# Kernel tuning notes

Hardware: AMD Instinct MI355X
Metric: run time of the kernel (lower is better)

Reference implementation:

```python
import jax, jax.numpy as jnp
import numpy as np

L, H, D, DH, DFF, V, P, T, R = 12, 12, 768, 64, 3072, 30522, 512, 2, 50
RAT_LAYER = 6  # original condition: 5 < idx < 7


def layer_norm(x, g, b, eps=1e-12):
    m = x.mean(-1, keepdims=True)
    v = ((x - m) ** 2).mean(-1, keepdims=True)
    return (x - m) / jnp.sqrt(v + eps) * g + b


def setup_inputs() -> dict:
    key = jax.random.key(0)
    ks = iter(jax.random.split(key, 20))
    def n(shape, s=0.02):
        return jax.random.normal(next(ks), shape, dtype=jnp.float32) * s
    inp = dict(
        input_ids=jax.random.randint(next(ks), (4, 512), 0, V, dtype=jnp.int32),
        relations=jax.random.randint(next(ks), (4, 512, 512), 0, R, dtype=jnp.int32),
        attention_mask=jnp.ones((4, 512), dtype=jnp.int32),
        word_emb=n((V, D)), pos_emb=n((P, D)), type_emb=n((T, D)),
        emb_ln_g=jnp.ones((D,)), emb_ln_b=jnp.zeros((D,)),
        Wq=n((L, D, D)), bq=jnp.zeros((L, D)), Wk=n((L, D, D)), bk=jnp.zeros((L, D)),
        Wv=n((L, D, D)), bv=jnp.zeros((L, D)), Wo=n((L, D, D)), bo=jnp.zeros((L, D)),
        ln1_g=jnp.ones((L, D)), ln1_b=jnp.zeros((L, D)),
        Wi=n((L, D, DFF)), bi=jnp.zeros((L, DFF)),
        Wf=n((L, DFF, D)), bf=jnp.zeros((L, D)),
        ln2_g=jnp.ones((L, D)), ln2_b=jnp.zeros((L, D)),
        key_rel=n((L, R, DH)), val_rel=n((L, R, DH)),
        pool_w=n((D, D)), pool_b=jnp.zeros((D,)),
    )
    return inp


def reference(input_ids, relations, attention_mask, word_emb, pos_emb, type_emb,
              emb_ln_g, emb_ln_b, Wq, bq, Wk, bk, Wv, bv, Wo, bo, ln1_g, ln1_b,
              Wi, bi, Wf, bf, ln2_g, ln2_b, key_rel, val_rel, pool_w, pool_b):
    B, S = input_ids.shape
    # BERT embeddings (token_type_ids = zeros as in module default)
    h = word_emb[input_ids] + pos_emb[jnp.arange(S)][None] + type_emb[0][None, None]
    h = layer_norm(h, emb_ln_g, emb_ln_b)
    ext_mask = (1.0 - attention_mask.astype(jnp.float32))[:, None, None, :] * -10000.0
    inv_sqrt_dh = np.float32(1.0 / np.sqrt(DH))
    for i in range(L):
        q = (h @ Wq[i] + bq[i]).reshape(B, S, H, DH).transpose(0, 2, 1, 3)
        k = (h @ Wk[i] + bk[i]).reshape(B, S, H, DH).transpose(0, 2, 1, 3)
        v = (h @ Wv[i] + bv[i]).reshape(B, S, H, DH).transpose(0, 2, 1, 3)
        scores = jnp.einsum('bhsd,bhtd->bhst', q, k)
        if i == RAT_LAYER:
            kr = key_rel[i][relations]            # [B,S,S,DH] gathered relation keys
            scores = scores + jnp.einsum('bhsd,bstd->bhst', q, kr)
        scores = scores * inv_sqrt_dh + ext_mask
        probs = jax.nn.softmax(scores, axis=-1)   # dropout = identity (eval)
        ctx = jnp.einsum('bhst,bhtd->bhsd', probs, v)
        if i == RAT_LAYER:
            vr = val_rel[i][relations]            # [B,S,S,DH] gathered relation values
            ctx = ctx + jnp.einsum('bhst,bstd->bhsd', probs, vr)
        ctx = ctx.transpose(0, 2, 1, 3).reshape(B, S, D)
        attn_out = layer_norm(ctx @ Wo[i] + bo[i] + h, ln1_g[i], ln1_b[i])
        ff = jax.nn.gelu(attn_out @ Wi[i] + bi[i], approximate=False)
        h = layer_norm(ff @ Wf[i] + bf[i] + attn_out, ln2_g[i], ln2_b[i])
    pooled = jnp.tanh(h[:, 0] @ pool_w + pool_b)
    return h, pooled
```

## Files before the change

kernel.cpp:

```cpp
#include <hip/hip_runtime.h>
#include <math.h>

typedef unsigned short u16;
typedef unsigned int   u32;
typedef __bf16  bf16x8 __attribute__((ext_vector_type(8)));
typedef float   f32x4  __attribute__((ext_vector_type(4)));
typedef u16     u16x8  __attribute__((ext_vector_type(8)));

__device__ __forceinline__ u16 f2bf(float f) {
  u32 u = __builtin_bit_cast(u32, f);
  u32 r = (u + 0x7fffu + ((u >> 16) & 1u)) >> 16;
  return (u16)r;
}
__device__ __forceinline__ float bf2f(u16 h) {
  u32 u = ((u32)h) << 16;
  return __builtin_bit_cast(float, u);
}
__device__ __forceinline__ void gload16(const void* g, void* l) {
  __builtin_amdgcn_global_load_lds((const __attribute__((address_space(1))) void*)g,
                                   (__attribute__((address_space(3))) void*)l, 16, 0, 0);
}
__device__ __forceinline__ bf16x8 ld_bf8(const u16* p) {
  u16x8 v = *(const u16x8*)p;
  return __builtin_bit_cast(bf16x8, v);
}
__device__ __forceinline__ f32x4 mfma16(bf16x8 a, bf16x8 b, f32x4 c) {
  return __builtin_amdgcn_mfma_f32_16x16x32_bf16(a, b, c, 0, 0, 0);
}

struct ConvP {
  const float *wq, *wk, *wv, *wo, *wi, *wf;
  u16 *oqkv, *oo, *oi, *of;
};
__global__ __launch_bounds__(256) void conv_weights(ConvP p) {
  int t = blockIdx.x;
  const float* in; u16* out; int K, N, tn, tk;
  if (t < 1728) { int wh = t / 576, tt = t % 576;
    in = wh==0 ? p.wq : (wh==1 ? p.wk : p.wv);
    out = p.oqkv + (size_t)wh * 768 * 768;
    K = 768; N = 768; tn = tt % 24; tk = tt / 24;
  } else if (t < 2304) { int tt = t - 1728; in = p.wo; out = p.oo; K=768;  N=768;  tn=tt%24; tk=tt/24; }
  else if (t < 4608)   { int tt = t - 2304; in = p.wi; out = p.oi; K=768;  N=3072; tn=tt%96; tk=tt/96; }
  else                 { int tt = t - 4608; in = p.wf; out = p.of; K=3072; N=768;  tn=tt%24; tk=tt/24; }
  int n0 = tn*32, k0 = tk*32;
  __shared__ float tile[32][33];
  int x = threadIdx.x, y = threadIdx.y;
  #pragma unroll
  for (int j = 0; j < 4; ++j)
    tile[y + j*8][x] = in[(size_t)(k0 + y + j*8) * N + n0 + x];
  __syncthreads();
  #pragma unroll
  for (int j = 0; j < 4; ++j)
    out[(size_t)(n0 + y + j*8) * K + k0 + x] = f2bf(tile[x][y + j*8]);
}

struct GP {
  const u16* A; const u16* B;
  int K, N;
  long sA, sB, sOut;
  const float* bias; const float* res;
  float* outF; u16* outB;
  const float* bq; const float* bk; const float* bv;
  u16* qO; u16* kO; u16* vO;
};

template<int BM, int BN, int WAVES, int EPI, int KS>
__global__ __launch_bounds__(WAVES*64) void gemm_bt(GP p) {
  constexpr int THREADS = WAVES * 64;
  constexpr int WC = WAVES / 2;
  constexpr int WM = BM / 2, WN = BN / WC, MR = WM / 16, NR = WN / 16;
  constexpr int AIT = BM * 64 / (THREADS * 8);
  constexpr int BIT = BN * 64 / (THREADS * 8);
  const int tid = threadIdx.x;
  const int wave = tid >> 6, lane = tid & 63;
  const int wr = wave / WC, wc = wave % WC;
  const int wm0 = wr * WM, wn0 = wc * WN;
  const int bn = blockIdx.x, bm = blockIdx.y, bz = blockIdx.z;
  const int K = p.K;
  const int kLen = K / KS;
  const int kBeg = (KS > 1) ? bz * kLen : 0;
  const u16* A  = p.A + ((KS > 1) ? 0 : (size_t)bz * p.sA);
  const u16* Bp = p.B + ((KS > 1) ? 0 : (size_t)bz * p.sB);
  const int rowA0 = bm * BM, colB0 = bn * BN;

  __shared__ __align__(16) u16 lds[(BM + BN) * 64];
  u16* Al = lds; u16* Bl = lds + BM * 64;

  f32x4 acc[MR][NR];
  #pragma unroll
  for (int i = 0; i < MR; ++i)
    #pragma unroll
    for (int j = 0; j < NR; ++j) acc[i][j] = f32x4{0.f,0.f,0.f,0.f};

  for (int kt = kBeg; kt < kBeg + kLen; kt += 64) {
    #pragma unroll
    for (int it = 0; it < AIT; ++it) {
      int e = tid * 8 + it * THREADS * 8;
      gload16(A + (size_t)(rowA0 + (e >> 6)) * K + kt + (e & 63), Al + e);
    }
    #pragma unroll
    for (int it = 0; it < BIT; ++it) {
      int e = tid * 8 + it * THREADS * 8;
      gload16(Bp + (size_t)(colB0 + (e >> 6)) * K + kt + (e & 63), Bl + e);
    }
    __syncthreads();
    #pragma unroll
    for (int ks = 0; ks < 2; ++ks) {
      bf16x8 av[MR]; bf16x8 bw[NR];
      #pragma unroll
      for (int mf = 0; mf < MR; ++mf)
        av[mf] = ld_bf8(Al + (wm0 + mf*16 + (lane&15))*64 + ks*32 + (lane>>4)*8);
      #pragma unroll
      for (int nf = 0; nf < NR; ++nf)
        bw[nf] = ld_bf8(Bl + (wn0 + nf*16 + (lane&15))*64 + ks*32 + (lane>>4)*8);
      #pragma unroll
      for (int mf = 0; mf < MR; ++mf)
        #pragma unroll
        for (int nf = 0; nf < NR; ++nf)
          acc[mf][nf] = mfma16(av[mf], bw[nf], acc[mf][nf]);
    }
    __syncthreads();
  }

  #pragma unroll
  for (int mf = 0; mf < MR; ++mf) {
    #pragma unroll
    for (int nf = 0; nf < NR; ++nf) {
      int col = colB0 + wn0 + nf*16 + (lane & 15);
      #pragma unroll
      for (int reg = 0; reg < 4; ++reg) {
        int row = rowA0 + wm0 + mf*16 + (lane >> 4)*4 + reg;
        float v = acc[mf][nf][reg];
        if constexpr (EPI == 0) {
          int wh = col / 768, cc = col % 768;
          int hh = cc >> 6, d = col & 63;
          int b = row >> 9, s = row & 511;
          const float* bias = wh==0 ? p.bq : (wh==1 ? p.bk : p.bv);
          u16 o = f2bf(v + bias[cc]);
          if (wh == 0)      p.qO[((((size_t)b*12 + hh)*512 + s) << 6) + d] = o;
          else if (wh == 1) p.kO[((((size_t)b*12 + hh)*512 + s) << 6) + d] = o;
          else              p.vO[((((size_t)b*12 + hh)*64  + d) << 9) + s] = o;
        } else if constexpr (EPI == 1) {
          int b = bz / 12, hh = bz % 12;
          p.outB[((size_t)(b*512 + row))*768 + hh*64 + col] = f2bf(v);
        } else if constexpr (EPI == 2) {
          p.outF[(size_t)bz * p.sOut + (size_t)row * p.N + col] = v;
        } else {
          float xg = v + p.bias[col];
          float gg = 0.5f * xg * (1.f + erff(xg * 0.70710678118f));
          p.outB[(size_t)row * p.N + col] = f2bf(gg);
        }
      }
    }
  }
}

__global__ __launch_bounds__(256) void attn_scores(
    const u16* __restrict__ q, const u16* __restrict__ k,
    const int* __restrict__ mask, u16* __restrict__ probs,
    const float* __restrict__ qr, const int* __restrict__ rel,
    float* __restrict__ wbins, int rat) {
  int st = blockIdx.x, hh = blockIdx.y, b = blockIdx.z;
  int tid = threadIdx.x, wave = tid >> 6, lane = tid & 63;
  size_t bh = (size_t)b * 12 + hh;
  const u16* qb = q + bh * 512 * 64;
  const u16* kb = k + bh * 512 * 64;

  f32x4 acc[2][8];
  #pragma unroll
  for (int i = 0; i < 2; ++i)
    #pragma unroll
    for (int j = 0; j < 8; ++j) acc[i][j] = f32x4{0.f,0.f,0.f,0.f};

  #pragma unroll
  for (int ks = 0; ks < 2; ++ks) {
    bf16x8 a0 = ld_bf8(qb + (size_t)(st*32      + (lane&15))*64 + ks*32 + (lane>>4)*8);
    bf16x8 a1 = ld_bf8(qb + (size_t)(st*32 + 16 + (lane&15))*64 + ks*32 + (lane>>4)*8);
    #pragma unroll
    for (int nf = 0; nf < 8; ++nf) {
      int t = wave*128 + nf*16 + (lane&15);
      bf16x8 bb = ld_bf8(kb + (size_t)t*64 + ks*32 + (lane>>4)*8);
      acc[0][nf] = mfma16(a0, bb, acc[0][nf]);
      acc[1][nf] = mfma16(a1, bb, acc[1][nf]);
    }
  }

  __shared__ float qlds[32][52];
  __shared__ float wlds[32][52];
  if (rat) {
    for (int i = tid; i < 32*52; i += 256) ((float*)wlds)[i] = 0.f;
    for (int i = tid; i < 32*50; i += 256) {
      int rr = i % 50, sr = i / 50;
      qlds[sr][rr] = qr[(bh*512 + st*32 + sr)*50 + rr];
    }
    __syncthreads();
    #pragma unroll
    for (int mf = 0; mf < 2; ++mf)
      #pragma unroll
      for (int nf = 0; nf < 8; ++nf) {
        int t = wave*128 + nf*16 + (lane&15);
        #pragma unroll
        for (int reg = 0; reg < 4; ++reg) {
          int rl = mf*16 + (lane>>4)*4 + reg;
          int rr = rel[((size_t)b*512 + st*32 + rl)*512 + t];
          acc[mf][nf][reg] += qlds[rl][rr];
        }
      }
  }

  #pragma unroll
  for (int nf = 0; nf < 8; ++nf) {
    int t = wave*128 + nf*16 + (lane&15);
    float em = -10000.f * (1.f - (float)mask[b*512 + t]);
    #pragma unroll
    for (int mf = 0; mf < 2; ++mf)
      #pragma unroll
      for (int reg = 0; reg < 4; ++reg)
        acc[mf][nf][reg] = acc[mf][nf][reg] * 0.125f + em;
  }

  __shared__ float red[4][32];
  __shared__ float gval[32];

  float rmax[2][4];
  #pragma unroll
  for (int mf = 0; mf < 2; ++mf)
    #pragma unroll
    for (int reg = 0; reg < 4; ++reg) {
      float m = -3.4e38f;
      #pragma unroll
      for (int nf = 0; nf < 8; ++nf) m = fmaxf(m, acc[mf][nf][reg]);
      #pragma unroll
      for (int o = 1; o < 16; o <<= 1) m = fmaxf(m, __shfl_xor(m, o));
      rmax[mf][reg] = m;
    }
  if ((lane & 15) == 0) {
    #pragma unroll
    for (int mf = 0; mf < 2; ++mf)
      #pragma unroll
      for (int reg = 0; reg < 4; ++reg)
        red[wave][mf*16 + (lane>>4)*4 + reg] = rmax[mf][reg];
  }
  __syncthreads();
  if (tid < 32)
    gval[tid] = fmaxf(fmaxf(red[0][tid], red[1][tid]), fmaxf(red[2][tid], red[3][tid]));
  __syncthreads();

  float rsum[2][4] = {{0,0,0,0},{0,0,0,0}};
  #pragma unroll
  for (int mf = 0; mf < 2; ++mf)
    #pragma unroll
    for (int reg = 0; reg < 4; ++reg) {
      int rl = mf*16 + (lane>>4)*4 + reg;
      float gm = gval[rl];
      #pragma unroll
      for (int nf = 0; nf < 8; ++nf) {
        float pv = __expf(acc[mf][nf][reg] - gm);
        acc[mf][nf][reg] = pv;
        rsum[mf][reg] += pv;
      }
    }
  #pragma unroll
  for (int mf = 0; mf < 2; ++mf)
    #pragma unroll
    for (int reg = 0; reg < 4; ++reg)
      #pragma unroll
      for (int o = 1; o < 16; o <<= 1) rsum[mf][reg] += __shfl_xor(rsum[mf][reg], o);
  __syncthreads();
  if ((lane & 15) == 0) {
    #pragma unroll
    for (int mf = 0; mf < 2; ++mf)
      #pragma unroll
      for (int reg = 0; reg < 4; ++reg)
        red[wave][mf*16 + (lane>>4)*4 + reg] = rsum[mf][reg];
  }
  __syncthreads();
  if (tid < 32)
    gval[tid] = red[0][tid] + red[1][tid] + red[2][tid] + red[3][tid];
  __syncthreads();

  #pragma unroll
  for (int mf = 0; mf < 2; ++mf)
    #pragma unroll
    for (int reg = 0; reg < 4; ++reg) {
      int rl = mf*16 + (lane>>4)*4 + reg;
      float inv = 1.f / gval[rl];
      size_t rowbase = (bh*512 + st*32 + rl) * 512;
      #pragma unroll
      for (int nf = 0; nf < 8; ++nf) {
        int t = wave*128 + nf*16 + (lane&15);
        float pval = acc[mf][nf][reg] * inv;
        probs[rowbase + t] = f2bf(pval);
        if (rat) {
          int rr = rel[((size_t)b*512 + st*32 + rl)*512 + t];
          atomicAdd(&wlds[rl][rr], pval);
        }
      }
    }
  if (rat) {
    __syncthreads();
    for (int i = tid; i < 32*50; i += 256) {
      int rr = i % 50, sr = i / 50;
      wbins[(bh*512 + st*32 + sr)*50 + rr] = wlds[sr][rr];
    }
  }
}

__global__ __launch_bounds__(256) void rat_qr(const u16* __restrict__ q,
    const float* __restrict__ kr, float* __restrict__ qr) {
  int idx = blockIdx.x * 256 + threadIdx.x;
  if (idx >= 24576 * 50) return;
  int r = idx % 50; size_t bhs = (size_t)idx / 50;
  const u16* qp = q + bhs * 64;
  const float* kp = kr + r * 64;
  float acc = 0.f;
  #pragma unroll
  for (int d = 0; d < 64; ++d) acc += bf2f(qp[d]) * kp[d];
  qr[idx] = acc;
}

__global__ __launch_bounds__(256) void rat_apply(const float* __restrict__ wbins,
    const float* __restrict__ vr, u16* __restrict__ ctx) {
  __shared__ float vrl[50*64];
  __shared__ float wl[32*50];
  int tid = threadIdx.x;
  int rows0 = blockIdx.x * 32;
  for (int i = tid; i < 50*64; i += 256) vrl[i] = vr[i];
  for (int i = tid; i < 32*50; i += 256) wl[i] = wbins[(size_t)rows0*50 + i];
  __syncthreads();
  int wave = tid >> 6, lane = tid & 63;
  #pragma unroll
  for (int i = 0; i < 8; ++i) {
    int r = wave*8 + i;
    size_t idx = (size_t)rows0 + r;
    float acc = 0.f;
    #pragma unroll
    for (int j = 0; j < 50; ++j) acc += wl[r*50 + j] * vrl[j*64 + lane];
    int s = (int)(idx & 511); size_t bh = idx >> 9;
    int b = (int)(bh / 12), hh = (int)(bh % 12);
    u16* cp = ctx + ((size_t)(b*512 + s))*768 + hh*64 + lane;
    *cp = f2bf(bf2f(*cp) + acc);
  }
}

__global__ __launch_bounds__(256) void embed_ln(const int* __restrict__ ids,
    const float* __restrict__ we, const float* __restrict__ pe, const float* __restrict__ te,
    const float* __restrict__ g, const float* __restrict__ b,
    float* __restrict__ hF, u16* __restrict__ hB) {
  int row = blockIdx.x, tid = threadIdx.x;
  int s = row & 511;
  int id = ids[row];
  float x[3];
  #pragma unroll
  for (int j = 0; j < 3; ++j) {
    int d = tid + j*256;
    x[j] = we[(size_t)id*768 + d] + pe[(size_t)s*768 + d] + te[d];
  }
  __shared__ float red[4];
  float sm = x[0] + x[1] + x[2];
  #pragma unroll
  for (int o = 32; o; o >>= 1) sm += __shfl_xor(sm, o);
  if (!(tid & 63)) red[tid >> 6] = sm;
  __syncthreads();
  float mean = (red[0]+red[1]+red[2]+red[3]) * (1.f/768.f);
  __syncthreads();
  float q = 0.f;
  #pragma unroll
  for (int j = 0; j < 3; ++j) { float d = x[j] - mean; q += d*d; }
  #pragma unroll
  for (int o = 32; o; o >>= 1) q += __shfl_xor(q, o);
  if (!(tid & 63)) red[tid >> 6] = q;
  __syncthreads();
  float inv = rsqrtf((red[0]+red[1]+red[2]+red[3]) * (1.f/768.f) + 1e-12f);
  #pragma unroll
  for (int j = 0; j < 3; ++j) {
    int d = tid + j*256;
    float y = (x[j] - mean) * inv * g[d] + b[d];
    hF[(size_t)row*768 + d] = y;
    hB[(size_t)row*768 + d] = f2bf(y);
  }
}

__global__ __launch_bounds__(256) void ln_fused(const float* __restrict__ p0,
    const float* __restrict__ p1, const float* __restrict__ p2, const float* __restrict__ p3,
    int np, const float* __restrict__ bias, const float* __restrict__ res,
    const float* __restrict__ g, const float* __restrict__ b,
    float* __restrict__ oF, u16* __restrict__ oB) {
  int row = blockIdx.x, tid = threadIdx.x;
  size_t base = (size_t)row * 768;
  float v[3];
  #pragma unroll
  for (int j = 0; j < 3; ++j) {
    int d = tid + j*256;
    float x = p0[base + d];
    if (np > 1) x += p1[base + d];
    if (np > 2) x += p2[base + d];
    if (np > 3) x += p3[base + d];
    v[j] = x + bias[d] + res[base + d];
  }
  __shared__ float red[4];
  float sm = v[0] + v[1] + v[2];
  #pragma unroll
  for (int o = 32; o; o >>= 1) sm += __shfl_xor(sm, o);
  if (!(tid & 63)) red[tid >> 6] = sm;
  __syncthreads();
  float mean = (red[0]+red[1]+red[2]+red[3]) * (1.f/768.f);
  __syncthreads();
  float q = 0.f;
  #pragma unroll
  for (int j = 0; j < 3; ++j) { float d = v[j] - mean; q += d*d; }
  #pragma unroll
  for (int o = 32; o; o >>= 1) q += __shfl_xor(q, o);
  if (!(tid & 63)) red[tid >> 6] = q;
  __syncthreads();
  float inv = rsqrtf((red[0]+red[1]+red[2]+red[3]) * (1.f/768.f) + 1e-12f);
  #pragma unroll
  for (int j = 0; j < 3; ++j) {
    int d = tid + j*256;
    float y = (v[j] - mean) * inv * g[d] + b[d];
    oF[base + d] = y;
    oB[base + d] = f2bf(y);
  }
}

__global__ __launch_bounds__(256) void pooler_k(const float* __restrict__ h,
    const float* __restrict__ w, const float* __restrict__ bias, float* __restrict__ out) {
  int b = blockIdx.x, tid = threadIdx.x;
  __shared__ float hr[768];
  for (int i = tid; i < 768; i += 256) hr[i] = h[((size_t)b*512)*768 + i];
  __syncthreads();
  float a0 = 0.f, a1 = 0.f, a2 = 0.f;
  for (int kk = 0; kk < 768; ++kk) {
    float hv = hr[kk];
    const float* wr = w + (size_t)kk*768;
    a0 += hv * wr[tid]; a1 += hv * wr[tid+256]; a2 += hv * wr[tid+512];
  }
  out[(size_t)b*768 + tid]       = tanhf(a0 + bias[tid]);
  out[(size_t)b*768 + tid + 256] = tanhf(a1 + bias[tid+256]);
  out[(size_t)b*768 + tid + 512] = tanhf(a2 + bias[tid+512]);
}

__global__ __launch_bounds__(256) void copy_out(const float* __restrict__ in, float* __restrict__ out) {
  size_t i = ((size_t)blockIdx.x * 256 + threadIdx.x) * 4;
  *(float4*)(out + i) = *(const float4*)(in + i);
}

extern "C" void kernel_launch(void* const* d_in, const int* in_sizes, int n_in,
                              void* d_out, int out_size, void* d_ws, size_t ws_size,
                              hipStream_t stream) {
  const int*   ids   = (const int*)d_in[0];
  const int*   rel   = (const int*)d_in[1];
  const int*   amask = (const int*)d_in[2];
  const float* we    = (const float*)d_in[3];
  const float* pe    = (const float*)d_in[4];
  const float* te    = (const float*)d_in[5];
  const float* eg    = (const float*)d_in[6];
  const float* ebb   = (const float*)d_in[7];
  const float* Wq    = (const float*)d_in[8];
  const float* bq    = (const float*)d_in[9];
  const float* Wk    = (const float*)d_in[10];
  const float* bk    = (const float*)d_in[11];
  const float* Wv    = (const float*)d_in[12];
  const float* bv    = (const float*)d_in[13];
  const float* Wo    = (const float*)d_in[14];
  const float* bo    = (const float*)d_in[15];
  const float* g1    = (const float*)d_in[16];
  const float* b1    = (const float*)d_in[17];
  const float* Wi    = (const float*)d_in[18];
  const float* bi    = (const float*)d_in[19];
  const float* Wf    = (const float*)d_in[20];
  const float* bfp   = (const float*)d_in[21];
  const float* g2    = (const float*)d_in[22];
  const float* b2    = (const float*)d_in[23];
  const float* krel  = (const float*)d_in[24];
  const float* vrel  = (const float*)d_in[25];
  const float* pwp   = (const float*)d_in[26];
  const float* pbp   = (const float*)d_in[27];
  (void)in_sizes; (void)n_in; (void)out_size; (void)ws_size;

  char* ws = (char*)d_ws;
  size_t off = 0;
  auto take = [&](size_t bytes) { char* p = ws + off; off += (bytes + 255) & ~(size_t)255; return p; };
  u16*   wqkv = (u16*)take((size_t)2304*768*2);
  u16*   wo_l = (u16*)take((size_t)768*768*2);
  u16*   wi_l = (u16*)take((size_t)3072*768*2);
  u16*   wf_l = (u16*)take((size_t)768*3072*2);
  float* hF   = (float*)take((size_t)2048*768*4);
  u16*   hB   = (u16*)take((size_t)2048*768*2);
  float* atF  = (float*)take((size_t)2048*768*4);
  u16*   atB  = (u16*)take((size_t)2048*768*2);
  u16*   qB   = (u16*)take((size_t)2048*768*2);
  u16*   kB   = (u16*)take((size_t)2048*768*2);
  u16*   vB   = (u16*)take((size_t)2048*768*2);
  u16*   ctxB = (u16*)take((size_t)2048*768*2);
  float* tmpF = (float*)take((size_t)4*2048*768*4);
  u16*   ffB  = (u16*)take((size_t)2048*3072*2);
  u16*   prB  = (u16*)take((size_t)48*512*512*2);
  float* qrF  = (float*)take((size_t)24576*50*4);
  float* wbF  = (float*)take((size_t)24576*50*4);
  const size_t PSTRIDE = (size_t)2048*768;

  embed_ln<<<2048, 256, 0, stream>>>(ids, we, pe, te, eg, ebb, hF, hB);

  for (int l = 0; l < 12; ++l) {
    ConvP cp{Wq + (size_t)l*768*768, Wk + (size_t)l*768*768, Wv + (size_t)l*768*768,
             Wo + (size_t)l*768*768, Wi + (size_t)l*768*3072, Wf + (size_t)l*3072*768,
             wqkv, wo_l, wi_l, wf_l};
    conv_weights<<<6912, dim3(32,8), 0, stream>>>(cp);

    GP pq{}; pq.A = hB; pq.B = wqkv; pq.K = 768; pq.N = 2304;
    pq.bq = bq + l*768; pq.bk = bk + l*768; pq.bv = bv + l*768;
    pq.qO = qB; pq.kO = kB; pq.vO = vB;
    gemm_bt<128,128,8,0,1><<<dim3(18,16,1), 512, 0, stream>>>(pq);

    int rat = (l == 6) ? 1 : 0;
    if (rat) rat_qr<<<4800, 256, 0, stream>>>(qB, krel + 6*50*64, qrF);
    attn_scores<<<dim3(16,12,4), 256, 0, stream>>>(qB, kB, amask, prB, qrF, rel, wbF, rat);

    GP pc{}; pc.A = prB; pc.B = vB; pc.K = 512; pc.N = 64;
    pc.sA = 512*512; pc.sB = 64*512; pc.outB = ctxB;
    gemm_bt<64,64,4,1,1><<<dim3(1,8,48), 256, 0, stream>>>(pc);
    if (rat) rat_apply<<<768, 256, 0, stream>>>(wbF, vrel + 6*50*64, ctxB);

    GP po{}; po.A = ctxB; po.B = wo_l; po.K = 768; po.N = 768; po.sOut = PSTRIDE;
    po.outF = tmpF;
    gemm_bt<64,128,4,2,2><<<dim3(6,32,2), 256, 0, stream>>>(po);
    ln_fused<<<2048, 256, 0, stream>>>(tmpF, tmpF + PSTRIDE, nullptr, nullptr, 2,
                                       bo + l*768, hF, g1 + l*768, b1 + l*768, atF, atB);

    GP pf1{}; pf1.A = atB; pf1.B = wi_l; pf1.K = 768; pf1.N = 3072;
    pf1.bias = bi + (size_t)l*3072; pf1.outB = ffB;
    gemm_bt<128,128,8,3,1><<<dim3(24,16,1), 512, 0, stream>>>(pf1);

    GP pf2{}; pf2.A = ffB; pf2.B = wf_l; pf2.K = 3072; pf2.N = 768; pf2.sOut = PSTRIDE;
    pf2.outF = tmpF;
    gemm_bt<64,128,4,2,4><<<dim3(6,32,4), 256, 0, stream>>>(pf2);
    ln_fused<<<2048, 256, 0, stream>>>(tmpF, tmpF + PSTRIDE, tmpF + 2*PSTRIDE, tmpF + 3*PSTRIDE, 4,
                                       bfp + l*768, atF, g2 + l*768, b2 + l*768, hF, hB);
  }

  copy_out<<<1536, 256, 0, stream>>>(hF, (float*)d_out);
  pooler_k<<<4, 256, 0, stream>>>(hF, pwp, pbp, (float*)d_out + (size_t)2048*768);
}
```

Measured before the change: 2.009 ms.

## Fuse probs@V into attention scores kernel, keeping probabilities in LDS

The attention kernel now stages each block's normalized 32x512 probability tile in LDS as bf16 and immediately computes the P·V product with MFMA, writing the context directly in [B,S,D] layout. This removes the global probability buffer (48x512x512 bf16) write and re-read, plus the separate batched GEMM launch. In exchange, each block uses about 33KB more LDS, which may reduce occupancy, and V is re-read from global by every row-tile block.

After: 1.984 ms. Within noise of the previous version (-1.2%).

```diff
diff --git a/kernel.cpp b/kernel.cpp
--- a/kernel.cpp
+++ b/kernel.cpp
@@ -140,9 +140,6 @@
           if (wh == 0)      p.qO[((((size_t)b*12 + hh)*512 + s) << 6) + d] = o;
           else if (wh == 1) p.kO[((((size_t)b*12 + hh)*512 + s) << 6) + d] = o;
           else              p.vO[((((size_t)b*12 + hh)*64  + d) << 9) + s] = o;
-        } else if constexpr (EPI == 1) {
-          int b = bz / 12, hh = bz % 12;
-          p.outB[((size_t)(b*512 + row))*768 + hh*64 + col] = f2bf(v);
         } else if constexpr (EPI == 2) {
           p.outF[(size_t)bz * p.sOut + (size_t)row * p.N + col] = v;
         } else {
@@ -155,9 +152,9 @@
   }
 }
 
-__global__ __launch_bounds__(256) void attn_scores(
-    const u16* __restrict__ q, const u16* __restrict__ k,
-    const int* __restrict__ mask, u16* __restrict__ probs,
+__global__ __launch_bounds__(256) void attn_fused(
+    const u16* __restrict__ q, const u16* __restrict__ k, const u16* __restrict__ v,
+    const int* __restrict__ mask, u16* __restrict__ ctx,
     const float* __restrict__ qr, const int* __restrict__ rel,
     float* __restrict__ wbins, int rat) {
   int st = blockIdx.x, hh = blockIdx.y, b = blockIdx.z;
@@ -166,6 +163,12 @@
   const u16* qb = q + bh * 512 * 64;
   const u16* kb = k + bh * 512 * 64;
 
+  __shared__ __align__(16) u16 plds[32 * 520];
+  __shared__ float qlds[32][52];
+  __shared__ float wlds[32][52];
+  __shared__ float red[4][32];
+  __shared__ float gval[32];
+
   f32x4 acc[2][8];
   #pragma unroll
   for (int i = 0; i < 2; ++i)
@@ -185,8 +188,6 @@
     }
   }
 
-  __shared__ float qlds[32][52];
-  __shared__ float wlds[32][52];
   if (rat) {
     for (int i = tid; i < 32*52; i += 256) ((float*)wlds)[i] = 0.f;
     for (int i = tid; i < 32*50; i += 256) {
@@ -219,9 +220,6 @@
         acc[mf][nf][reg] = acc[mf][nf][reg] * 0.125f + em;
   }
 
-  __shared__ float red[4][32];
-  __shared__ float gval[32];
-
   float rmax[2][4];
   #pragma unroll
   for (int mf = 0; mf < 2; ++mf)
@@ -285,12 +283,11 @@
     for (int reg = 0; reg < 4; ++reg) {
       int rl = mf*16 + (lane>>4)*4 + reg;
       float inv = 1.f / gval[rl];
-      size_t rowbase = (bh*512 + st*32 + rl) * 512;
       #pragma unroll
       for (int nf = 0; nf < 8; ++nf) {
         int t = wave*128 + nf*16 + (lane&15);
         float pval = acc[mf][nf][reg] * inv;
-        probs[rowbase + t] = f2bf(pval);
+        plds[rl*520 + t] = f2bf(pval);
         if (rat) {
           int rr = rel[((size_t)b*512 + st*32 + rl)*512 + t];
           atomicAdd(&wlds[rl][rr], pval);
@@ -303,6 +300,30 @@
       int rr = i % 50, sr = i / 50;
       wbins[(bh*512 + st*32 + sr)*50 + rr] = wlds[sr][rr];
     }
+  }
+  __syncthreads();
+
+  const u16* vb = v + bh * 64 * 512;
+  int mt = wave >> 1, nb = wave & 1;
+  int lrow = mt*16 + (lane & 15);
+  int g = lane >> 4;
+  f32x4 c0 = f32x4{0.f,0.f,0.f,0.f}, c1 = f32x4{0.f,0.f,0.f,0.f};
+  #pragma unroll
+  for (int kt = 0; kt < 16; ++kt) {
+    bf16x8 pa = ld_bf8(plds + lrow*520 + kt*32 + g*8);
+    bf16x8 b0 = ld_bf8(vb + (size_t)(nb*16      + (lane&15))*512 + kt*32 + g*8);
+    bf16x8 b1 = ld_bf8(vb + (size_t)((nb+2)*16  + (lane&15))*512 + kt*32 + g*8);
+    c0 = mfma16(pa, b0, c0);
+    c1 = mfma16(pa, b1, c1);
+  }
+  #pragma unroll
+  for (int reg = 0; reg < 4; ++reg) {
+    int s = st*32 + mt*16 + g*4 + reg;
+    int d0 = nb*16 + (lane & 15);
+    int d1 = (nb+2)*16 + (lane & 15);
+    size_t rb = ((size_t)(b*512 + s))*768 + hh*64;
+    ctx[rb + d0] = f2bf(c0[reg]);
+    ctx[rb + d1] = f2bf(c1[reg]);
   }
 }
 
@@ -495,7 +516,6 @@
   u16*   ctxB = (u16*)take((size_t)2048*768*2);
   float* tmpF = (float*)take((size_t)4*2048*768*4);
   u16*   ffB  = (u16*)take((size_t)2048*3072*2);
-  u16*   prB  = (u16*)take((size_t)48*512*512*2);
   float* qrF  = (float*)take((size_t)24576*50*4);
   float* wbF  = (float*)take((size_t)24576*50*4);
   const size_t PSTRIDE = (size_t)2048*768;
@@ -515,11 +535,7 @@
 
     int rat = (l == 6) ? 1 : 0;
     if (rat) rat_qr<<<4800, 256, 0, stream>>>(qB, krel + 6*50*64, qrF);
-    attn_scores<<<dim3(16,12,4), 256, 0, stream>>>(qB, kB, amask, prB, qrF, rel, wbF, rat);
-
-    GP pc{}; pc.A = prB; pc.B = vB; pc.K = 512; pc.N = 64;
-    pc.sA = 512*512; pc.sB = 64*512; pc.outB = ctxB;
-    gemm_bt<64,64,4,1,1><<<dim3(1,8,48), 256, 0, stream>>>(pc);
+    attn_fused<<<dim3(16,12,4), 256, 0, stream>>>(qB, kB, vB, amask, ctxB, qrF, rel, wbF, rat);
     if (rat) rat_apply<<<768, 256, 0, stream>>>(wbF, vrel + 6*50*64, ctxB);
 
     GP po{}; po.A = ctxB; po.B = wo_l; po.K = 768; po.N = 768; po.sOut = PSTRIDE;
```

## Fuse attention scores, softmax and PV into one kernel with probs in LDS

Applied to the files above, without the earlier changes.

Replaces the separate score/softmax kernel and the batched P·V GEMM with one kernel per 64-query tile. Each wave owns 16 full rows, so the row max and sum need only a wave shuffle, and probabilities stay in LDS as bf16 instead of round-tripping a 48x512x512 global buffer. It also remaps block IDs so the tiles of one head share an XCD, and packs relation indices into registers for the RAT layer. The costs are higher register and LDS pressure per block (32 accumulator tiles, about 66KB of probs) and fewer blocks (384), which may lower occupancy.

New measurement: 2.145 ms. +6.8%, slower.

```diff
diff --git a/kernel.cpp b/kernel.cpp
--- a/kernel.cpp
+++ b/kernel.cpp
@@ -140,9 +140,6 @@
           if (wh == 0)      p.qO[((((size_t)b*12 + hh)*512 + s) << 6) + d] = o;
           else if (wh == 1) p.kO[((((size_t)b*12 + hh)*512 + s) << 6) + d] = o;
           else              p.vO[((((size_t)b*12 + hh)*64  + d) << 9) + s] = o;
-        } else if constexpr (EPI == 1) {
-          int b = bz / 12, hh = bz % 12;
-          p.outB[((size_t)(b*512 + row))*768 + hh*64 + col] = f2bf(v);
         } else if constexpr (EPI == 2) {
           p.outF[(size_t)bz * p.sOut + (size_t)row * p.N + col] = v;
         } else {
@@ -155,153 +152,139 @@
   }
 }
 
-__global__ __launch_bounds__(256) void attn_scores(
-    const u16* __restrict__ q, const u16* __restrict__ k,
-    const int* __restrict__ mask, u16* __restrict__ probs,
+template<int RAT>
+__global__ __launch_bounds__(256, RAT ? 1 : 2) void attn_fused2(
+    const u16* __restrict__ q, const u16* __restrict__ k, const u16* __restrict__ v,
+    const int* __restrict__ mask, u16* __restrict__ ctx,
     const float* __restrict__ qr, const int* __restrict__ rel,
-    float* __restrict__ wbins, int rat) {
-  int st = blockIdx.x, hh = blockIdx.y, b = blockIdx.z;
-  int tid = threadIdx.x, wave = tid >> 6, lane = tid & 63;
-  size_t bh = (size_t)b * 12 + hh;
+    float* __restrict__ wbins) {
+  const int bid = blockIdx.x;
+  const int xcd = bid & 7, slot = bid >> 3;
+  const int head = xcd * 6 + (slot >> 3);
+  const int st   = slot & 7;
+  const int b = head / 12, hh = head % 12;
+  const int tid = threadIdx.x, wave = tid >> 6, lane = tid & 63;
+  const size_t bh = (size_t)head;
   const u16* qb = q + bh * 512 * 64;
   const u16* kb = k + bh * 512 * 64;
-
-  f32x4 acc[2][8];
-  #pragma unroll
-  for (int i = 0; i < 2; ++i)
-    #pragma unroll
-    for (int j = 0; j < 8; ++j) acc[i][j] = f32x4{0.f,0.f,0.f,0.f};
-
-  #pragma unroll
-  for (int ks = 0; ks < 2; ++ks) {
-    bf16x8 a0 = ld_bf8(qb + (size_t)(st*32      + (lane&15))*64 + ks*32 + (lane>>4)*8);
-    bf16x8 a1 = ld_bf8(qb + (size_t)(st*32 + 16 + (lane&15))*64 + ks*32 + (lane>>4)*8);
-    #pragma unroll
-    for (int nf = 0; nf < 8; ++nf) {
-      int t = wave*128 + nf*16 + (lane&15);
-      bf16x8 bb = ld_bf8(kb + (size_t)t*64 + ks*32 + (lane>>4)*8);
-      acc[0][nf] = mfma16(a0, bb, acc[0][nf]);
-      acc[1][nf] = mfma16(a1, bb, acc[1][nf]);
-    }
-  }
-
-  __shared__ float qlds[32][52];
-  __shared__ float wlds[32][52];
-  if (rat) {
-    for (int i = tid; i < 32*52; i += 256) ((float*)wlds)[i] = 0.f;
-    for (int i = tid; i < 32*50; i += 256) {
+  const u16* vb = v + bh * 64 * 512;
+
+  __shared__ __align__(16) u16 plds[64 * 520];
+  __shared__ float em_lds[512];
+  __shared__ float l_lds[64];
+  extern __shared__ float dyn_unused[];
+
+  __shared__ float qlds[RAT ? 64 : 1][RAT ? 52 : 1];
+  __shared__ float wlds[RAT ? 64 : 1][RAT ? 52 : 1];
+
+  for (int i = tid; i < 512; i += 256)
+    em_lds[i] = -10000.f * (1.f - (float)mask[b*512 + i]);
+  if constexpr (RAT) {
+    for (int i = tid; i < 64*52; i += 256) ((float*)wlds)[i] = 0.f;
+    for (int i = tid; i < 64*50; i += 256) {
       int rr = i % 50, sr = i / 50;
-      qlds[sr][rr] = qr[(bh*512 + st*32 + sr)*50 + rr];
-    }
-    __syncthreads();
-    #pragma unroll
-    for (int mf = 0; mf < 2; ++mf)
+      qlds[sr][rr] = qr[(bh*512 + st*64 + sr)*50 + rr];
+    }
+  }
+  __syncthreads();
+
+  const int qrow = st*64 + wave*16 + (lane & 15);
+  bf16x8 aq0 = ld_bf8(qb + (size_t)qrow*64 +      (lane>>4)*8);
+  bf16x8 aq1 = ld_bf8(qb + (size_t)qrow*64 + 32 + (lane>>4)*8);
+
+  f32x4 acc[32];
+  #pragma unroll
+  for (int t = 0; t < 32; ++t) acc[t] = f32x4{0.f,0.f,0.f,0.f};
+
+  #pragma unroll
+  for (int t = 0; t < 32; ++t) {
+    const u16* kr = kb + (size_t)(t*16 + (lane&15))*64 + (lane>>4)*8;
+    bf16x8 b0 = ld_bf8(kr);
+    bf16x8 b1 = ld_bf8(kr + 32);
+    acc[t] = mfma16(aq0, b0, acc[t]);
+    acc[t] = mfma16(aq1, b1, acc[t]);
+  }
+
+  u32 rr4[RAT ? 32 : 1];
+  if constexpr (RAT) {
+    #pragma unroll
+    for (int t = 0; t < 32; ++t) {
+      int tt = t*16 + (lane&15);
+      u32 pack = 0;
       #pragma unroll
-      for (int nf = 0; nf < 8; ++nf) {
-        int t = wave*128 + nf*16 + (lane&15);
-        #pragma unroll
-        for (int reg = 0; reg < 4; ++reg) {
-          int rl = mf*16 + (lane>>4)*4 + reg;
-          int rr = rel[((size_t)b*512 + st*32 + rl)*512 + t];
-          acc[mf][nf][reg] += qlds[rl][rr];
-        }
+      for (int reg = 0; reg < 4; ++reg) {
+        int lq = wave*16 + (lane>>4)*4 + reg;
+        int rr = rel[((size_t)b*512 + st*64 + lq)*512 + tt];
+        pack |= (u32)rr << (8*reg);
+        acc[t][reg] += qlds[lq][rr];
       }
-  }
-
-  #pragma unroll
-  for (int nf = 0; nf < 8; ++nf) {
-    int t = wave*128 + nf*16 + (lane&15);
-    float em = -10000.f * (1.f - (float)mask[b*512 + t]);
-    #pragma unroll
-    for (int mf = 0; mf < 2; ++mf)
-      #pragma unroll
-      for (int reg = 0; reg < 4; ++reg)
-        acc[mf][nf][reg] = acc[mf][nf][reg] * 0.125f + em;
-  }
-
-  __shared__ float red[4][32];
-  __shared__ float gval[32];
-
-  float rmax[2][4];
-  #pragma unroll
-  for (int mf = 0; mf < 2; ++mf)
+      rr4[t] = pack;
+    }
+  }
+
+  #pragma unroll
+  for (int t = 0; t < 32; ++t) {
+    float em = em_lds[t*16 + (lane&15)];
+    #pragma unroll
+    for (int reg = 0; reg < 4; ++reg)
+      acc[t][reg] = acc[t][reg] * 0.125f + em;
+  }
+
+  #pragma unroll
+  for (int reg = 0; reg < 4; ++reg) {
+    const int lq = wave*16 + (lane>>4)*4 + reg;
+    float m = acc[0][reg];
+    #pragma unroll
+    for (int t = 1; t < 32; ++t) m = fmaxf(m, acc[t][reg]);
+    #pragma unroll
+    for (int o = 1; o < 16; o <<= 1) m = fmaxf(m, __shfl_xor(m, o));
+    float s = 0.f;
+    #pragma unroll
+    for (int t = 0; t < 32; ++t) {
+      float e = __expf(acc[t][reg] - m);
+      acc[t][reg] = e;
+      s += e;
+      if constexpr (RAT) {
+        int rr = (rr4[t] >> (8*reg)) & 255;
+        atomicAdd(&wlds[lq][rr], e);
+      }
+    }
+    #pragma unroll
+    for (int o = 1; o < 16; o <<= 1) s += __shfl_xor(s, o);
+    if ((lane & 15) == 0) l_lds[lq] = s;
+    float inv = 1.f / s;
+    #pragma unroll
+    for (int t = 0; t < 32; ++t)
+      plds[(size_t)lq*520 + t*16 + (lane&15)] = f2bf(acc[t][reg] * inv);
+  }
+  __syncthreads();
+
+  if constexpr (RAT) {
+    for (int i = tid; i < 64*50; i += 256) {
+      int rr = i % 50, sr = i / 50;
+      wbins[(bh*512 + st*64 + sr)*50 + rr] = wlds[sr][rr] / l_lds[sr];
+    }
+  }
+
+  f32x4 cpv[4];
+  #pragma unroll
+  for (int dt = 0; dt < 4; ++dt) cpv[dt] = f32x4{0.f,0.f,0.f,0.f};
+  #pragma unroll
+  for (int ks = 0; ks < 16; ++ks) {
+    bf16x8 pa = ld_bf8(plds + (size_t)(wave*16 + (lane&15))*520 + ks*32 + (lane>>4)*8);
+    #pragma unroll
+    for (int dt = 0; dt < 4; ++dt) {
+      bf16x8 bv_ = ld_bf8(vb + (size_t)(dt*16 + (lane&15))*512 + ks*32 + (lane>>4)*8);
+      cpv[dt] = mfma16(pa, bv_, cpv[dt]);
+    }
+  }
+  #pragma unroll
+  for (int dt = 0; dt < 4; ++dt) {
     #pragma unroll
     for (int reg = 0; reg < 4; ++reg) {
-      float m = -3.4e38f;
-      #pragma unroll
-      for (int nf = 0; nf < 8; ++nf) m = fmaxf(m, acc[mf][nf][reg]);
-      #pragma unroll
-      for (int o = 1; o < 16; o <<= 1) m = fmaxf(m, __shfl_xor(m, o));
-      rmax[mf][reg] = m;
-    }
-  if ((lane & 15) == 0) {
-    #pragma unroll
-    for (int mf = 0; mf < 2; ++mf)
-      #pragma unroll
-      for (int reg = 0; reg < 4; ++reg)
-        red[wave][mf*16 + (lane>>4)*4 + reg] = rmax[mf][reg];
-  }
-  __syncthreads();
-  if (tid < 32)
-    gval[tid] = fmaxf(fmaxf(red[0][tid], red[1][tid]), fmaxf(red[2][tid], red[3][tid]));
-  __syncthreads();
-
-  float rsum[2][4] = {{0,0,0,0},{0,0,0,0}};
-  #pragma unroll
-  for (int mf = 0; mf < 2; ++mf)
-    #pragma unroll
-    for (int reg = 0; reg < 4; ++reg) {
-      int rl = mf*16 + (lane>>4)*4 + reg;
-      float gm = gval[rl];
-      #pragma unroll
-      for (int nf = 0; nf < 8; ++nf) {
-        float pv = __expf(acc[mf][nf][reg] - gm);
-        acc[mf][nf][reg] = pv;
-        rsum[mf][reg] += pv;
-      }
-    }
-  #pragma unroll
-  for (int mf = 0; mf < 2; ++mf)
-    #pragma unroll
-    for (int reg = 0; reg < 4; ++reg)
-      #pragma unroll
-      for (int o = 1; o < 16; o <<= 1) rsum[mf][reg] += __shfl_xor(rsum[mf][reg], o);
-  __syncthreads();
-  if ((lane & 15) == 0) {
-    #pragma unroll
-    for (int mf = 0; mf < 2; ++mf)
-      #pragma unroll
-      for (int reg = 0; reg < 4; ++reg)
-        red[wave][mf*16 + (lane>>4)*4 + reg] = rsum[mf][reg];
-  }
-  __syncthreads();
-  if (tid < 32)
-    gval[tid] = red[0][tid] + red[1][tid] + red[2][tid] + red[3][tid];
-  __syncthreads();
-
-  #pragma unroll
-  for (int mf = 0; mf < 2; ++mf)
-    #pragma unroll
-    for (int reg = 0; reg < 4; ++reg) {
-      int rl = mf*16 + (lane>>4)*4 + reg;
-      float inv = 1.f / gval[rl];
-      size_t rowbase = (bh*512 + st*32 + rl) * 512;
-      #pragma unroll
-      for (int nf = 0; nf < 8; ++nf) {
-        int t = wave*128 + nf*16 + (lane&15);
-        float pval = acc[mf][nf][reg] * inv;
-        probs[rowbase + t] = f2bf(pval);
-        if (rat) {
-          int rr = rel[((size_t)b*512 + st*32 + rl)*512 + t];
-          atomicAdd(&wlds[rl][rr], pval);
-        }
-      }
-    }
-  if (rat) {
-    __syncthreads();
-    for (int i = tid; i < 32*50; i += 256) {
-      int rr = i % 50, sr = i / 50;
-      wbins[(bh*512 + st*32 + sr)*50 + rr] = wlds[sr][rr];
+      int qg = st*64 + wave*16 + (lane>>4)*4 + reg;
+      int d  = dt*16 + (lane&15);
+      ctx[((size_t)(b*512 + qg))*768 + hh*64 + d] = f2bf(cpv[dt][reg]);
     }
   }
 }
@@ -495,7 +478,6 @@
   u16*   ctxB = (u16*)take((size_t)2048*768*2);
   float* tmpF = (float*)take((size_t)4*2048*768*4);
   u16*   ffB  = (u16*)take((size_t)2048*3072*2);
-  u16*   prB  = (u16*)take((size_t)48*512*512*2);
   float* qrF  = (float*)take((size_t)24576*50*4);
   float* wbF  = (float*)take((size_t)24576*50*4);
   const size_t PSTRIDE = (size_t)2048*768;
@@ -513,14 +495,13 @@
     pq.qO = qB; pq.kO = kB; pq.vO = vB;
     gemm_bt<128,128,8,0,1><<<dim3(18,16,1), 512, 0, stream>>>(pq);
 
-    int rat = (l == 6) ? 1 : 0;
-    if (rat) rat_qr<<<4800, 256, 0, stream>>>(qB, krel + 6*50*64, qrF);
-    attn_scores<<<dim3(16,12,4), 256, 0, stream>>>(qB, kB, amask, prB, qrF, rel, wbF, rat);
-
-    GP pc{}; pc.A = prB; pc.B = vB; pc.K = 512; pc.N = 64;
-    pc.sA = 512*512; pc.sB = 64*512; pc.outB = ctxB;
-    gemm_bt<64,64,4,1,1><<<dim3(1,8,48), 256, 0, stream>>>(pc);
-    if (rat) rat_apply<<<768, 256, 0, stream>>>(wbF, vrel + 6*50*64, ctxB);
+    if (l == 6) {
+      rat_qr<<<4800, 256, 0, stream>>>(qB, krel + 6*50*64, qrF);
+      attn_fused2<1><<<384, 256, 0, stream>>>(qB, kB, vB, amask, ctxB, qrF, rel, wbF);
+      rat_apply<<<768, 256, 0, stream>>>(wbF, vrel + 6*50*64, ctxB);
+    } else {
+      attn_fused2<0><<<384, 256, 0, stream>>>(qB, kB, vB, amask, ctxB, qrF, rel, wbF);
+    }
 
     GP po{}; po.A = ctxB; po.B = wo_l; po.K = 768; po.N = 768; po.sOut = PSTRIDE;
     po.outF = tmpF;
```

## Stage Q/K tiles in LDS with 64-row blocks and templated RAT path

Applied to the files above, without the earlier changes.

The attention-scores kernel now handles 64 query rows per block instead of 32. It stages the Q tile and the full K for the head into LDS via global_load_lds, then runs the MFMAs from shared memory rather than from direct global loads. The mask bias is precomputed into LDS, and the RAT branch is a template parameter, so non-RAT layers compile without it. This cuts redundant global K reads across blocks, at the cost of about 74KB of LDS per block, which limits occupancy, and fewer blocks (384).

New measurement: 2.215 ms. 1.1x slower.

```diff
diff --git a/kernel.cpp b/kernel.cpp
--- a/kernel.cpp
+++ b/kernel.cpp
@@ -155,153 +155,160 @@
   }
 }
 
-__global__ __launch_bounds__(256) void attn_scores(
+template<int RAT>
+__global__ __launch_bounds__(256) void scores_sm(
     const u16* __restrict__ q, const u16* __restrict__ k,
     const int* __restrict__ mask, u16* __restrict__ probs,
     const float* __restrict__ qr, const int* __restrict__ rel,
-    float* __restrict__ wbins, int rat) {
-  int st = blockIdx.x, hh = blockIdx.y, b = blockIdx.z;
-  int tid = threadIdx.x, wave = tid >> 6, lane = tid & 63;
-  size_t bh = (size_t)b * 12 + hh;
-  const u16* qb = q + bh * 512 * 64;
-  const u16* kb = k + bh * 512 * 64;
-
-  f32x4 acc[2][8];
-  #pragma unroll
-  for (int i = 0; i < 2; ++i)
-    #pragma unroll
-    for (int j = 0; j < 8; ++j) acc[i][j] = f32x4{0.f,0.f,0.f,0.f};
+    float* __restrict__ wbins) {
+  const int head = blockIdx.x;
+  const int bm   = blockIdx.y;
+  const int b = head / 12;
+  const int row0 = bm * 64;
+  const int tid = threadIdx.x, wc = tid >> 6, lane = tid & 63;
+
+  __shared__ __align__(16) u16 lds[(64 + 512) * 64];
+  u16* Al = lds;
+  u16* Bl = lds + 64*64;
+  __shared__ float em_lds[512];
+  __shared__ float red[64][4];
+  __shared__ float gmax[64], gsum[64];
+
+  for (int i = tid; i < 512; i += 256)
+    em_lds[i] = -10000.f * (1.f - (float)mask[b*512 + i]);
+
+  const u16* qb = q + (size_t)head * 512 * 64;
+  const u16* kb = k + (size_t)head * 512 * 64;
+  #pragma unroll
+  for (int it = 0; it < 2; ++it) {
+    int e = tid*8 + it*2048;
+    gload16(qb + (size_t)(row0 + (e>>6))*64 + (e&63), Al + e);
+  }
+  #pragma unroll
+  for (int it = 0; it < 16; ++it) {
+    int e = tid*8 + it*2048;
+    gload16(kb + (size_t)(e>>6)*64 + (e&63), Bl + e);
+  }
+  __syncthreads();
+
+  f32x4 acc[4][8];
+  #pragma unroll
+  for (int mf = 0; mf < 4; ++mf)
+    #pragma unroll
+    for (int nf = 0; nf < 8; ++nf) acc[mf][nf] = f32x4{0.f,0.f,0.f,0.f};
 
   #pragma unroll
   for (int ks = 0; ks < 2; ++ks) {
-    bf16x8 a0 = ld_bf8(qb + (size_t)(st*32      + (lane&15))*64 + ks*32 + (lane>>4)*8);
-    bf16x8 a1 = ld_bf8(qb + (size_t)(st*32 + 16 + (lane&15))*64 + ks*32 + (lane>>4)*8);
-    #pragma unroll
-    for (int nf = 0; nf < 8; ++nf) {
-      int t = wave*128 + nf*16 + (lane&15);
-      bf16x8 bb = ld_bf8(kb + (size_t)t*64 + ks*32 + (lane>>4)*8);
-      acc[0][nf] = mfma16(a0, bb, acc[0][nf]);
-      acc[1][nf] = mfma16(a1, bb, acc[1][nf]);
-    }
-  }
-
-  __shared__ float qlds[32][52];
-  __shared__ float wlds[32][52];
-  if (rat) {
-    for (int i = tid; i < 32*52; i += 256) ((float*)wlds)[i] = 0.f;
-    for (int i = tid; i < 32*50; i += 256) {
+    bf16x8 av[4]; bf16x8 bw[8];
+    #pragma unroll
+    for (int mf = 0; mf < 4; ++mf)
+      av[mf] = ld_bf8(Al + (mf*16 + (lane&15))*64 + ks*32 + (lane>>4)*8);
+    #pragma unroll
+    for (int nf = 0; nf < 8; ++nf)
+      bw[nf] = ld_bf8(Bl + (wc*128 + nf*16 + (lane&15))*64 + ks*32 + (lane>>4)*8);
+    #pragma unroll
+    for (int mf = 0; mf < 4; ++mf)
+      #pragma unroll
+      for (int nf = 0; nf < 8; ++nf)
+        acc[mf][nf] = mfma16(av[mf], bw[nf], acc[mf][nf]);
+  }
+  __syncthreads();
+
+  float* wlds = (float*)lds;
+  float* qlds = (float*)(lds + 32768);
+  if constexpr (RAT) {
+    for (int i = tid; i < 64*52; i += 256) wlds[i] = 0.f;
+    for (int i = tid; i < 64*50; i += 256) {
       int rr = i % 50, sr = i / 50;
-      qlds[sr][rr] = qr[(bh*512 + st*32 + sr)*50 + rr];
+      qlds[sr*52 + rr] = qr[((size_t)head*512 + row0 + sr)*50 + rr];
     }
     __syncthreads();
     #pragma unroll
-    for (int mf = 0; mf < 2; ++mf)
+    for (int mf = 0; mf < 4; ++mf)
       #pragma unroll
       for (int nf = 0; nf < 8; ++nf) {
-        int t = wave*128 + nf*16 + (lane&15);
+        int col = wc*128 + nf*16 + (lane&15);
         #pragma unroll
         for (int reg = 0; reg < 4; ++reg) {
-          int rl = mf*16 + (lane>>4)*4 + reg;
-          int rr = rel[((size_t)b*512 + st*32 + rl)*512 + t];
-          acc[mf][nf][reg] += qlds[rl][rr];
+          int row = mf*16 + (lane>>4)*4 + reg;
+          int rr = rel[((size_t)(b*512 + row0 + row))*512 + col];
+          acc[mf][nf][reg] += qlds[row*52 + rr];
         }
       }
   }
 
   #pragma unroll
-  for (int nf = 0; nf < 8; ++nf) {
-    int t = wave*128 + nf*16 + (lane&15);
-    float em = -10000.f * (1.f - (float)mask[b*512 + t]);
-    #pragma unroll
-    for (int mf = 0; mf < 2; ++mf)
+  for (int mf = 0; mf < 4; ++mf)
+    #pragma unroll
+    for (int nf = 0; nf < 8; ++nf) {
+      float em = em_lds[wc*128 + nf*16 + (lane&15)];
       #pragma unroll
       for (int reg = 0; reg < 4; ++reg)
         acc[mf][nf][reg] = acc[mf][nf][reg] * 0.125f + em;
-  }
-
-  __shared__ float red[4][32];
-  __shared__ float gval[32];
-
-  float rmax[2][4];
-  #pragma unroll
-  for (int mf = 0; mf < 2; ++mf)
+    }
+
+  #pragma unroll
+  for (int mf = 0; mf < 4; ++mf)
     #pragma unroll
     for (int reg = 0; reg < 4; ++reg) {
-      float m = -3.4e38f;
-      #pragma unroll
-      for (int nf = 0; nf < 8; ++nf) m = fmaxf(m, acc[mf][nf][reg]);
+      int row = mf*16 + (lane>>4)*4 + reg;
+      float m = acc[mf][0][reg];
+      #pragma unroll
+      for (int nf = 1; nf < 8; ++nf) m = fmaxf(m, acc[mf][nf][reg]);
       #pragma unroll
       for (int o = 1; o < 16; o <<= 1) m = fmaxf(m, __shfl_xor(m, o));
-      rmax[mf][reg] = m;
-    }
-  if ((lane & 15) == 0) {
-    #pragma unroll
-    for (int mf = 0; mf < 2; ++mf)
-      #pragma unroll
-      for (int reg = 0; reg < 4; ++reg)
-        red[wave][mf*16 + (lane>>4)*4 + reg] = rmax[mf][reg];
-  }
-  __syncthreads();
-  if (tid < 32)
-    gval[tid] = fmaxf(fmaxf(red[0][tid], red[1][tid]), fmaxf(red[2][tid], red[3][tid]));
-  __syncthreads();
-
-  float rsum[2][4] = {{0,0,0,0},{0,0,0,0}};
-  #pragma unroll
-  for (int mf = 0; mf < 2; ++mf)
+      if ((lane & 15) == 0) red[row][wc] = m;
+    }
+  __syncthreads();
+  if (tid < 64)
+    gmax[tid] = fmaxf(fmaxf(red[tid][0], red[tid][1]), fmaxf(red[tid][2], red[tid][3]));
+  __syncthreads();
+
+  #pragma unroll
+  for (int mf = 0; mf < 4; ++mf)
     #pragma unroll
     for (int reg = 0; reg < 4; ++reg) {
-      int rl = mf*16 + (lane>>4)*4 + reg;
-      float gm = gval[rl];
+      int row = mf*16 + (lane>>4)*4 + reg;
+      float gm = gmax[row];
+      float s = 0.f;
       #pragma unroll
       for (int nf = 0; nf < 8; ++nf) {
-        float pv = __expf(acc[mf][nf][reg] - gm);
-        acc[mf][nf][reg] = pv;
-        rsum[mf][reg] += pv;
+        float e = __expf(acc[mf][nf][reg] - gm);
+        acc[mf][nf][reg] = e;
+        s += e;
       }
-    }
-  #pragma unroll
-  for (int mf = 0; mf < 2; ++mf)
-    #pragma unroll
-    for (int reg = 0; reg < 4; ++reg)
-      #pragma unroll
-      for (int o = 1; o < 16; o <<= 1) rsum[mf][reg] += __shfl_xor(rsum[mf][reg], o);
-  __syncthreads();
-  if ((lane & 15) == 0) {
-    #pragma unroll
-    for (int mf = 0; mf < 2; ++mf)
-      #pragma unroll
-      for (int reg = 0; reg < 4; ++reg)
-        red[wave][mf*16 + (lane>>4)*4 + reg] = rsum[mf][reg];
-  }
-  __syncthreads();
-  if (tid < 32)
-    gval[tid] = red[0][tid] + red[1][tid] + red[2][tid] + red[3][tid];
-  __syncthreads();
-
-  #pragma unroll
-  for (int mf = 0; mf < 2; ++mf)
+      #pragma unroll
+      for (int o = 1; o < 16; o <<= 1) s += __shfl_xor(s, o);
+      if ((lane & 15) == 0) red[row][wc] = s;
+    }
+  __syncthreads();
+  if (tid < 64)
+    gsum[tid] = red[tid][0] + red[tid][1] + red[tid][2] + red[tid][3];
+  __syncthreads();
+
+  #pragma unroll
+  for (int mf = 0; mf < 4; ++mf)
     #pragma unroll
     for (int reg = 0; reg < 4; ++reg) {
-      int rl = mf*16 + (lane>>4)*4 + reg;
-      float inv = 1.f / gval[rl];
-      size_t rowbase = (bh*512 + st*32 + rl) * 512;
+      int row = mf*16 + (lane>>4)*4 + reg;
+      float inv = 1.f / gsum[row];
+      size_t rowbase = ((size_t)head*512 + row0 + row) * 512;
       #pragma unroll
       for (int nf = 0; nf < 8; ++nf) {
-        int t = wave*128 + nf*16 + (lane&15);
+        int col = wc*128 + nf*16 + (lane&15);
         float pval = acc[mf][nf][reg] * inv;
-        probs[rowbase + t] = f2bf(pval);
-        if (rat) {
-          int rr = rel[((size_t)b*512 + st*32 + rl)*512 + t];
-          atomicAdd(&wlds[rl][rr], pval);
+        probs[rowbase + col] = f2bf(pval);
+        if constexpr (RAT) {
+          int rr = rel[((size_t)(b*512 + row0 + row))*512 + col];
+          atomicAdd(&wlds[row*52 + rr], pval);
         }
       }
     }
-  if (rat) {
+  if constexpr (RAT) {
     __syncthreads();
-    for (int i = tid; i < 32*50; i += 256) {
+    for (int i = tid; i < 64*50; i += 256) {
       int rr = i % 50, sr = i / 50;
-      wbins[(bh*512 + st*32 + sr)*50 + rr] = wlds[sr][rr];
+      wbins[((size_t)head*512 + row0 + sr)*50 + rr] = wlds[sr*52 + rr];
     }
   }
 }
@@ -513,14 +520,17 @@
     pq.qO = qB; pq.kO = kB; pq.vO = vB;
     gemm_bt<128,128,8,0,1><<<dim3(18,16,1), 512, 0, stream>>>(pq);
 
-    int rat = (l == 6) ? 1 : 0;
-    if (rat) rat_qr<<<4800, 256, 0, stream>>>(qB, krel + 6*50*64, qrF);
-    attn_scores<<<dim3(16,12,4), 256, 0, stream>>>(qB, kB, amask, prB, qrF, rel, wbF, rat);
+    if (l == 6) {
+      rat_qr<<<4800, 256, 0, stream>>>(qB, krel + 6*50*64, qrF);
+      scores_sm<1><<<dim3(48,8), 256, 0, stream>>>(qB, kB, amask, prB, qrF, rel, wbF);
+    } else {
+      scores_sm<0><<<dim3(48,8), 256, 0, stream>>>(qB, kB, amask, prB, qrF, rel, wbF);
+    }
 
     GP pc{}; pc.A = prB; pc.B = vB; pc.K = 512; pc.N = 64;
-    pc.sA = 512*512; pc.sB = 64*512; pc.outB = ctxB;
+    pc.sA = (long)512*512; pc.sB = 64*512; pc.outB = ctxB;
     gemm_bt<64,64,4,1,1><<<dim3(1,8,48), 256, 0, stream>>>(pc);
-    if (rat) rat_apply<<<768, 256, 0, stream>>>(wbF, vrel + 6*50*64, ctxB);
+    if (l == 6) rat_apply<<<768, 256, 0, stream>>>(wbF, vrel + 6*50*64, ctxB);
 
     GP po{}; po.A = ctxB; po.B = wo_l; po.K = 768; po.N = 768; po.sOut = PSTRIDE;
     po.outF = tmpF;
```
